# Performance work log

Measured on AMD Instinct MI355X. Metric: run time of the kernel, lower is better.

The kernel has to match this reference:

```python
import jax, jax.numpy as jnp
import numpy as np

N, C, K = 200000, 128, 27  # active voxels, channels, 3x3x3 kernel taps
EPS = 1e-5  # torch LayerNorm default


def setup_inputs() -> dict:
    key = jax.random.key(0)
    ks = jax.random.split(key, 8)
    feats = jax.random.normal(ks[0], (N, C), dtype=jnp.float32)
    # plan-based gather map: neighbor row index per voxel per kernel tap
    neighbor_idx = jax.random.randint(ks[1], (N, K), 0, N, dtype=jnp.int32)
    # sparse conv weights: one [C_in, C_out] slice per kernel offset
    conv_w = jax.random.normal(ks[2], (K, C, C), dtype=jnp.float32) * (1.0 / np.sqrt(K * C))
    conv_b = jax.random.normal(ks[3], (C,), dtype=jnp.float32) * 0.02
    # torch.nn.Linear(C, C): weight [out, in], y = x @ W^T + b
    lin_w = jax.random.normal(ks[4], (C, C), dtype=jnp.float32) * (1.0 / np.sqrt(C))
    lin_b = jax.random.normal(ks[5], (C,), dtype=jnp.float32) * 0.02
    ln_w = 1.0 + 0.02 * jax.random.normal(ks[6], (C,), dtype=jnp.float32)
    ln_b = 0.02 * jax.random.normal(ks[7], (C,), dtype=jnp.float32)
    return {
        "feats": feats, "neighbor_idx": neighbor_idx,
        "conv_w": conv_w, "conv_b": conv_b,
        "lin_w": lin_w, "lin_b": lin_b,
        "ln_w": ln_w, "ln_b": ln_b,
    }


def _sparse_conv(feats, neighbor_idx, conv_w, conv_b):
    # Stream over the 27 kernel taps: gather [N,C] then GEMM with the tap's
    # [C,C] slice; never materialize the [N,27,C] gathered tensor.
    def step(acc, tap):
        idx_k, w_k = tap  # idx_k: [N], w_k: [C, C]
        return acc + feats[idx_k] @ w_k, None

    acc0 = jnp.zeros((feats.shape[0], conv_w.shape[2]), dtype=feats.dtype)
    out, _ = jax.lax.scan(step, acc0, (neighbor_idx.T, conv_w))
    return out + conv_b


def reference(feats, neighbor_idx, conv_w, conv_b, lin_w, lin_b, ln_w, ln_b):
    x = _sparse_conv(feats, neighbor_idx, conv_w, conv_b)   # [N, C]
    x = x @ lin_w.T + lin_b                                  # Linear
    mu = jnp.mean(x, axis=-1, keepdims=True)                 # LayerNorm
    var = jnp.mean(jnp.square(x - mu), axis=-1, keepdims=True)
    x = (x - mu) * jax.lax.rsqrt(var + EPS) * ln_w + ln_b
    return x
```

## Files before the change

### kernel.cpp

```cpp
#include <hip/hip_runtime.h>
#include <hip/hip_bf16.h>
#include <stdint.h>

#define N_ROWS 200000
#define C_DIM  128
#define TAPS   27
#define EPS    1e-5f

typedef __attribute__((ext_vector_type(8)))  short  short8;
typedef __attribute__((ext_vector_type(16))) float  floatx16;

#if __has_builtin(__builtin_amdgcn_make_buffer_rsrc) && __has_builtin(__builtin_amdgcn_raw_buffer_load_b128)
#define GATHER_SC0 1
#else
#define GATHER_SC0 0
#endif

__device__ __forceinline__ unsigned int f2bf(float f) {
  union { float f; unsigned int u; } v; v.f = f;
  unsigned int r = v.u + 0x7FFFu + ((v.u >> 16) & 1u);
  return r >> 16;
}

__device__ __forceinline__ void glds16(const unsigned short* g, unsigned short* l) {
  __builtin_amdgcn_global_load_lds(
      (const __attribute__((address_space(1))) unsigned int*)g,
      (__attribute__((address_space(3))) unsigned int*)l, 16, 0, 0);
}

#if GATHER_SC0
__device__ __forceinline__ short8 ld16sc0(__amdgpu_buffer_rsrc_t r, int voff) {
  return __builtin_bit_cast(short8,
      __builtin_amdgcn_raw_buffer_load_b128(r, voff, 0, 1));
}
#endif

__global__ __launch_bounds__(256) void k_cast(const float* __restrict__ in,
                                              unsigned short* __restrict__ out, int n8) {
  int i = blockIdx.x * 256 + threadIdx.x;
  if (i >= n8) return;
  const float4* p = (const float4*)in + (size_t)i * 2;
  float4 a = p[0], b = p[1];
  uint4 v;
  v.x = f2bf(a.x) | (f2bf(a.y) << 16);
  v.y = f2bf(a.z) | (f2bf(a.w) << 16);
  v.z = f2bf(b.x) | (f2bf(b.y) << 16);
  v.w = f2bf(b.z) | (f2bf(b.w) << 16);
  *(uint4*)(out + (size_t)i * 8) = v;
}

__global__ __launch_bounds__(256) void k_tr(const int* __restrict__ in,
                                            int* __restrict__ outT) {
  __shared__ int t[1728];
  const int tile = blockIdx.x;
  const int* src = in + (size_t)tile * 1728;
  for (int e = threadIdx.x; e < 1728; e += 256) t[e] = src[e];
  __syncthreads();
  const int base = tile * 64;
  for (int o = threadIdx.x; o < 1728; o += 256) {
    int k = o >> 6, r = o & 63;
    outT[(size_t)k * N_ROWS + base + r] = t[r * 27 + k];
  }
}

__global__ __launch_bounds__(256) void k_fold(const float* __restrict__ conv_w,
                                              const float* __restrict__ lin_w,
                                              const float* __restrict__ conv_b,
                                              const float* __restrict__ lin_b,
                                              unsigned short* __restrict__ wfrag,
                                              float* __restrict__ biasf) {
  __shared__ float lwT[128 * 128];
  for (int e = threadIdx.x; e < 16384; e += 256) {
    int co = e >> 7, t = e & 127;
    lwT[t * 128 + (co ^ (t & 31))] = lin_w[e];
  }
  __syncthreads();

  int id = blockIdx.x * 256 + threadIdx.x;
  const int NW = TAPS * 4 * 8 * 64;
  if (id < NW) {
    int l  = id & 63;
    int s  = (id >> 6) & 7;
    int nt = (id >> 9) & 3;
    int k  = id >> 11;
    int ci0 = s * 16 + (l >> 5) * 8;
    int co  = nt * 32 + (l & 31);
    const float* cw = conv_w + ((size_t)(k * 128 + ci0)) * 128;
    float acc[8] = {0, 0, 0, 0, 0, 0, 0, 0};
    for (int t = 0; t < 128; ++t) {
      float lv = lwT[t * 128 + (co ^ (t & 31))];
#pragma unroll
      for (int j = 0; j < 8; ++j) acc[j] += cw[j * 128 + t] * lv;
    }
    uint4 v;
    v.x = f2bf(acc[0]) | (f2bf(acc[1]) << 16);
    v.y = f2bf(acc[2]) | (f2bf(acc[3]) << 16);
    v.z = f2bf(acc[4]) | (f2bf(acc[5]) << 16);
    v.w = f2bf(acc[6]) | (f2bf(acc[7]) << 16);
    *(uint4*)(wfrag + (size_t)id * 8) = v;
  } else if (id < NW + 128) {
    int co = id - NW;
    float s = lin_b[co];
    for (int t = 0; t < 128; ++t) s += conv_b[t] * lwT[t * 128 + (co ^ (t & 31))];
    biasf[co] = s;
  }
}

__global__ __launch_bounds__(512, 4) void k_main(const unsigned short* __restrict__ featsB,
                                                 const int* __restrict__ ntab,
                                                 const int nrs, const int nts,
                                                 const unsigned short* __restrict__ wfrag,
                                                 const float* __restrict__ biasf,
                                                 const float* __restrict__ lnw,
                                                 const float* __restrict__ lnb,
                                                 float* __restrict__ out) {
  __shared__ unsigned short ldsB[2][16384];

  const int tid = threadIdx.x;
  const int l   = tid & 63;
  const int w   = tid >> 6;
  const int l31 = l & 31;
  const int lh  = l >> 5;
  const int row0w = blockIdx.x * 256 + w * 32;
  const int gr  = row0w + l31;
  const int grc = (gr < N_ROWS) ? gr : 0;
  const int* np = ntab + (size_t)grc * nrs;

#if GATHER_SC0
  __amdgpu_buffer_rsrc_t rsrc = __builtin_amdgcn_make_buffer_rsrc(
      (void*)featsB, (short)0, N_ROWS * C_DIM * 2, 0x00020000);
#endif

  floatx16 acc0 = {0.f}, acc1 = {0.f}, acc2 = {0.f}, acc3 = {0.f};

  {
    const unsigned short* src = wfrag + (size_t)tid * 8;
    unsigned short* dst = &ldsB[0][w * 512];
#pragma unroll
    for (int r = 0; r < 4; ++r) glds16(src + r * 4096, dst + r * 4096);
  }
  int nid = np[0];

  for (int k = 0; k < TAPS; ++k) {
    const int cur = k & 1;
    if (k + 1 < TAPS) {
      const unsigned short* src = wfrag + (size_t)(k + 1) * 16384 + (size_t)tid * 8;
      unsigned short* dst = &ldsB[cur ^ 1][w * 512];
#pragma unroll
      for (int r = 0; r < 4; ++r) glds16(src + r * 4096, dst + r * 4096);
      __builtin_amdgcn_s_waitcnt(0xF74);
    } else {
      __builtin_amdgcn_s_waitcnt(0xF70);
    }
    __builtin_amdgcn_s_barrier();

#if GATHER_SC0
    const int voff = ((int)(unsigned)nid << 8) + (lh << 4);
    short8 a0 = ld16sc0(rsrc, voff);
    short8 a1 = ld16sc0(rsrc, voff + 32);
    short8 a2 = ld16sc0(rsrc, voff + 64);
    short8 a3 = ld16sc0(rsrc, voff + 96);
    short8 a4 = ld16sc0(rsrc, voff + 128);
    short8 a5 = ld16sc0(rsrc, voff + 160);
    short8 a6 = ld16sc0(rsrc, voff + 192);
    short8 a7 = ld16sc0(rsrc, voff + 224);
#else
    const short8* ap = (const short8*)(featsB + (size_t)(unsigned)nid * 128 + lh * 8);
    short8 a0 = ap[0],  a1 = ap[2],  a2 = ap[4],  a3 = ap[6];
    short8 a4 = ap[8],  a5 = ap[10], a6 = ap[12], a7 = ap[14];
#endif
    int nid_next = (k + 1 < TAPS) ? np[(k + 1) * nts] : 0;

    const unsigned short* bb = &ldsB[cur][l * 8];
#pragma unroll
    for (int s = 0; s < 8; ++s) {
      short8 av = (s == 0) ? a0 : (s == 1) ? a1 : (s == 2) ? a2 : (s == 3) ? a3
                : (s == 4) ? a4 : (s == 5) ? a5 : (s == 6) ? a6 : a7;
      short8 b0 = *(const short8*)(bb + (0 * 8 + s) * 512);
      short8 b1 = *(const short8*)(bb + (1 * 8 + s) * 512);
      short8 b2 = *(const short8*)(bb + (2 * 8 + s) * 512);
      short8 b3 = *(const short8*)(bb + (3 * 8 + s) * 512);
      acc0 = __builtin_amdgcn_mfma_f32_32x32x16_bf16(av, b0, acc0, 0, 0, 0);
      acc1 = __builtin_amdgcn_mfma_f32_32x32x16_bf16(av, b1, acc1, 0, 0, 0);
      acc2 = __builtin_amdgcn_mfma_f32_32x32x16_bf16(av, b2, acc2, 0, 0, 0);
      acc3 = __builtin_amdgcn_mfma_f32_32x32x16_bf16(av, b3, acc3, 0, 0, 0);
    }
    __builtin_amdgcn_s_barrier();
    nid = nid_next;
  }

  float b0 = biasf[l31], b1 = biasf[32 + l31], b2 = biasf[64 + l31], b3 = biasf[96 + l31];
  float g0 = lnw[l31],   g1 = lnw[32 + l31],   g2 = lnw[64 + l31],   g3 = lnw[96 + l31];
  float c0 = lnb[l31],   c1 = lnb[32 + l31],   c2 = lnb[64 + l31],   c3 = lnb[96 + l31];

#pragma unroll
  for (int r = 0; r < 16; ++r) {
    float x0 = acc0[r] + b0, x1 = acc1[r] + b1, x2 = acc2[r] + b2, x3 = acc3[r] + b3;
    float s = x0 + x1 + x2 + x3;
    float q = x0 * x0 + x1 * x1 + x2 * x2 + x3 * x3;
#pragma unroll
    for (int off = 16; off >= 1; off >>= 1) {
      s += __shfl_xor(s, off, 64);
      q += __shfl_xor(q, off, 64);
    }
    float mu  = s * (1.0f / 128.0f);
    float var = q * (1.0f / 128.0f) - mu * mu;
    float rs  = rsqrtf(var + EPS);
    int row   = (r & 3) + 8 * (r >> 2) + 4 * lh;
    int grow  = row0w + row;
    if (grow < N_ROWS) {
      float* o = out + (size_t)grow * 128;
      o[l31]      = (x0 - mu) * rs * g0 + c0;
      o[32 + l31] = (x1 - mu) * rs * g1 + c1;
      o[64 + l31] = (x2 - mu) * rs * g2 + c2;
      o[96 + l31] = (x3 - mu) * rs * g3 + c3;
    }
  }
}

extern "C" void kernel_launch(void* const* d_in, const int* in_sizes, int n_in,
                              void* d_out, int out_size, void* d_ws, size_t ws_size,
                              hipStream_t stream) {
  const float* feats  = (const float*)d_in[0];
  const int*   nidx   = (const int*)d_in[1];
  const float* conv_w = (const float*)d_in[2];
  const float* conv_b = (const float*)d_in[3];
  const float* lin_w  = (const float*)d_in[4];
  const float* lin_b  = (const float*)d_in[5];
  const float* ln_w   = (const float*)d_in[6];
  const float* ln_b   = (const float*)d_in[7];
  float* out = (float*)d_out;

  unsigned short* featsB = (unsigned short*)d_ws;
  unsigned short* wfrag  = (unsigned short*)((char*)d_ws + 51200000);
  float*          biasf  = (float*)((char*)d_ws + 51200000 + 884736);
  int*            nidxT  = (int*)((char*)d_ws + 51200000 + 884736 + 512);

  const size_t ws_need_tr = 51200000ULL + 884736ULL + 512ULL + 21600000ULL;
  const bool use_tr = (ws_size >= ws_need_tr);

  int n8 = N_ROWS * C_DIM / 8;
  k_cast<<<(n8 + 255) / 256, 256, 0, stream>>>(feats, featsB, n8);
  k_fold<<<(TAPS * 2048 + 128 + 255) / 256, 256, 0, stream>>>(conv_w, lin_w, conv_b, lin_b,
                                                              wfrag, biasf);
  if (use_tr) k_tr<<<N_ROWS / 64, 256, 0, stream>>>(nidx, nidxT);

  k_main<<<(N_ROWS + 255) / 256, 512, 0, stream>>>(
      featsB,
      use_tr ? (const int*)nidxT : nidx,
      use_tr ? 1 : TAPS,
      use_tr ? N_ROWS : 1,
      wfrag, biasf, ln_w, ln_b, out);
}
```

Before: 511.7 us.

## Shrink main block to 4 waves and stream half-tap weight slices through LDS

The main kernel drops from 512 to 256 threads per block (128 rows per block), and the weight fragments are reorganized into half-tap chunks (K split into two halves of 64) so each LDS buffer holds 16 KB instead of 32 KB. The tap loop now alternates between two half-buffers, prefetching the next half while computing the current one, with explicit sched_barriers around the s_barriers. The aim is to cut LDS footprint so more blocks fit per CU and to overlap weight loads with MFMA work. In exchange each block does twice as many barriers per tap, and weight traffic per row doubles because blocks are smaller.

```diff
diff --git a/kernel.cpp b/kernel.cpp
--- a/kernel.cpp
+++ b/kernel.cpp
@@ -15,6 +15,9 @@
 #else
 #define GATHER_SC0 0
 #endif
+
+#define SBAR()  __builtin_amdgcn_s_barrier()
+#define SCHED() __builtin_amdgcn_sched_barrier(0)
 
 __device__ __forceinline__ unsigned int f2bf(float f) {
   union { float f; unsigned int u; } v; v.f = f;
@@ -77,12 +80,14 @@
   __syncthreads();
 
   int id = blockIdx.x * 256 + threadIdx.x;
-  const int NW = TAPS * 4 * 8 * 64;
+  const int NW = TAPS * 2 * 4 * 4 * 64;
   if (id < NW) {
     int l  = id & 63;
-    int s  = (id >> 6) & 7;
-    int nt = (id >> 9) & 3;
+    int sh = (id >> 6) & 3;
+    int nt = (id >> 8) & 3;
+    int h  = (id >> 10) & 1;
     int k  = id >> 11;
+    int s  = h * 4 + sh;
     int ci0 = s * 16 + (l >> 5) * 8;
     int co  = nt * 32 + (l & 31);
     const float* cw = conv_w + ((size_t)(k * 128 + ci0)) * 128;
@@ -106,7 +111,7 @@
   }
 }
 
-__global__ __launch_bounds__(512, 4) void k_main(const unsigned short* __restrict__ featsB,
+__global__ __launch_bounds__(256, 4) void k_main(const unsigned short* __restrict__ featsB,
                                                  const int* __restrict__ ntab,
                                                  const int nrs, const int nts,
                                                  const unsigned short* __restrict__ wfrag,
@@ -114,14 +119,14 @@
                                                  const float* __restrict__ lnw,
                                                  const float* __restrict__ lnb,
                                                  float* __restrict__ out) {
-  __shared__ unsigned short ldsB[2][16384];
+  __shared__ unsigned short ldsB[2][8192];
 
   const int tid = threadIdx.x;
   const int l   = tid & 63;
   const int w   = tid >> 6;
   const int l31 = l & 31;
   const int lh  = l >> 5;
-  const int row0w = blockIdx.x * 256 + w * 32;
+  const int row0w = blockIdx.x * 128 + w * 32;
   const int gr  = row0w + l31;
   const int grc = (gr < N_ROWS) ? gr : 0;
   const int* np = ntab + (size_t)grc * nrs;
@@ -137,55 +142,89 @@
     const unsigned short* src = wfrag + (size_t)tid * 8;
     unsigned short* dst = &ldsB[0][w * 512];
 #pragma unroll
-    for (int r = 0; r < 4; ++r) glds16(src + r * 4096, dst + r * 4096);
+    for (int r = 0; r < 4; ++r) glds16(src + r * 2048, dst + r * 2048);
   }
   int nid = np[0];
-
-  for (int k = 0; k < TAPS; ++k) {
-    const int cur = k & 1;
-    if (k + 1 < TAPS) {
-      const unsigned short* src = wfrag + (size_t)(k + 1) * 16384 + (size_t)tid * 8;
-      unsigned short* dst = &ldsB[cur ^ 1][w * 512];
-#pragma unroll
-      for (int r = 0; r < 4; ++r) glds16(src + r * 4096, dst + r * 4096);
-      __builtin_amdgcn_s_waitcnt(0xF74);
-    } else {
-      __builtin_amdgcn_s_waitcnt(0xF70);
-    }
-    __builtin_amdgcn_s_barrier();
+  short8 a0, a1, a2, a3, a4, a5, a6, a7;
+
+  for (int t = 0; t < TAPS; ++t) {
+    {
+      const unsigned short* src = wfrag + (size_t)(2 * t + 1) * 8192 + (size_t)tid * 8;
+      unsigned short* dst = &ldsB[1][w * 512];
+#pragma unroll
+      for (int r = 0; r < 4; ++r) glds16(src + r * 2048, dst + r * 2048);
+    }
+    SCHED();
+    __builtin_amdgcn_s_waitcnt(0xF74);
+    SCHED();
+    SBAR();
+    SCHED();
 
 #if GATHER_SC0
     const int voff = ((int)(unsigned)nid << 8) + (lh << 4);
-    short8 a0 = ld16sc0(rsrc, voff);
-    short8 a1 = ld16sc0(rsrc, voff + 32);
-    short8 a2 = ld16sc0(rsrc, voff + 64);
-    short8 a3 = ld16sc0(rsrc, voff + 96);
-    short8 a4 = ld16sc0(rsrc, voff + 128);
-    short8 a5 = ld16sc0(rsrc, voff + 160);
-    short8 a6 = ld16sc0(rsrc, voff + 192);
-    short8 a7 = ld16sc0(rsrc, voff + 224);
+    a0 = ld16sc0(rsrc, voff);
+    a1 = ld16sc0(rsrc, voff + 32);
+    a2 = ld16sc0(rsrc, voff + 64);
+    a3 = ld16sc0(rsrc, voff + 96);
+    a4 = ld16sc0(rsrc, voff + 128);
+    a5 = ld16sc0(rsrc, voff + 160);
+    a6 = ld16sc0(rsrc, voff + 192);
+    a7 = ld16sc0(rsrc, voff + 224);
 #else
     const short8* ap = (const short8*)(featsB + (size_t)(unsigned)nid * 128 + lh * 8);
-    short8 a0 = ap[0],  a1 = ap[2],  a2 = ap[4],  a3 = ap[6];
-    short8 a4 = ap[8],  a5 = ap[10], a6 = ap[12], a7 = ap[14];
-#endif
-    int nid_next = (k + 1 < TAPS) ? np[(k + 1) * nts] : 0;
-
-    const unsigned short* bb = &ldsB[cur][l * 8];
-#pragma unroll
-    for (int s = 0; s < 8; ++s) {
-      short8 av = (s == 0) ? a0 : (s == 1) ? a1 : (s == 2) ? a2 : (s == 3) ? a3
-                : (s == 4) ? a4 : (s == 5) ? a5 : (s == 6) ? a6 : a7;
-      short8 b0 = *(const short8*)(bb + (0 * 8 + s) * 512);
-      short8 b1 = *(const short8*)(bb + (1 * 8 + s) * 512);
-      short8 b2 = *(const short8*)(bb + (2 * 8 + s) * 512);
-      short8 b3 = *(const short8*)(bb + (3 * 8 + s) * 512);
-      acc0 = __builtin_amdgcn_mfma_f32_32x32x16_bf16(av, b0, acc0, 0, 0, 0);
-      acc1 = __builtin_amdgcn_mfma_f32_32x32x16_bf16(av, b1, acc1, 0, 0, 0);
-      acc2 = __builtin_amdgcn_mfma_f32_32x32x16_bf16(av, b2, acc2, 0, 0, 0);
-      acc3 = __builtin_amdgcn_mfma_f32_32x32x16_bf16(av, b3, acc3, 0, 0, 0);
-    }
-    __builtin_amdgcn_s_barrier();
+    a0 = ap[0];  a1 = ap[2];  a2 = ap[4];  a3 = ap[6];
+    a4 = ap[8];  a5 = ap[10]; a6 = ap[12]; a7 = ap[14];
+#endif
+    int nid_next = (t + 1 < TAPS) ? np[(t + 1) * nts] : 0;
+
+    {
+      const unsigned short* bb = &ldsB[0][l * 8];
+#pragma unroll
+      for (int sh = 0; sh < 4; ++sh) {
+        short8 av = (sh == 0) ? a0 : (sh == 1) ? a1 : (sh == 2) ? a2 : a3;
+        short8 b0 = *(const short8*)(bb + (0 * 4 + sh) * 512);
+        short8 b1 = *(const short8*)(bb + (1 * 4 + sh) * 512);
+        short8 b2 = *(const short8*)(bb + (2 * 4 + sh) * 512);
+        short8 b3 = *(const short8*)(bb + (3 * 4 + sh) * 512);
+        acc0 = __builtin_amdgcn_mfma_f32_32x32x16_bf16(av, b0, acc0, 0, 0, 0);
+        acc1 = __builtin_amdgcn_mfma_f32_32x32x16_bf16(av, b1, acc1, 0, 0, 0);
+        acc2 = __builtin_amdgcn_mfma_f32_32x32x16_bf16(av, b2, acc2, 0, 0, 0);
+        acc3 = __builtin_amdgcn_mfma_f32_32x32x16_bf16(av, b3, acc3, 0, 0, 0);
+      }
+    }
+    SCHED();
+    SBAR();
+    SCHED();
+
+    if (t + 1 < TAPS) {
+      const unsigned short* src = wfrag + (size_t)(2 * t + 2) * 8192 + (size_t)tid * 8;
+      unsigned short* dst = &ldsB[0][w * 512];
+#pragma unroll
+      for (int r = 0; r < 4; ++r) glds16(src + r * 2048, dst + r * 2048);
+    }
+    SCHED();
+    SBAR();
+    SCHED();
+    {
+      const unsigned short* bb = &ldsB[1][l * 8];
+#pragma unroll
+      for (int sh = 0; sh < 4; ++sh) {
+        short8 av = (sh == 0) ? a4 : (sh == 1) ? a5 : (sh == 2) ? a6 : a7;
+        short8 b0 = *(const short8*)(bb + (0 * 4 + sh) * 512);
+        short8 b1 = *(const short8*)(bb + (1 * 4 + sh) * 512);
+        short8 b2 = *(const short8*)(bb + (2 * 4 + sh) * 512);
+        short8 b3 = *(const short8*)(bb + (3 * 4 + sh) * 512);
+        acc0 = __builtin_amdgcn_mfma_f32_32x32x16_bf16(av, b0, acc0, 0, 0, 0);
+        acc1 = __builtin_amdgcn_mfma_f32_32x32x16_bf16(av, b1, acc1, 0, 0, 0);
+        acc2 = __builtin_amdgcn_mfma_f32_32x32x16_bf16(av, b2, acc2, 0, 0, 0);
+        acc3 = __builtin_amdgcn_mfma_f32_32x32x16_bf16(av, b3, acc3, 0, 0, 0);
+      }
+    }
+    if (t + 1 < TAPS) {
+      SCHED();
+      SBAR();
+      SCHED();
+    }
     nid = nid_next;
   }
 
@@ -245,7 +284,7 @@
                                                               wfrag, biasf);
   if (use_tr) k_tr<<<N_ROWS / 64, 256, 0, stream>>>(nidx, nidxT);
 
-  k_main<<<(N_ROWS + 255) / 256, 512, 0, stream>>>(
+  k_main<<<(N_ROWS + 127) / 128, 256, 0, stream>>>(
       featsB,
       use_tr ? (const int*)nidxT : nidx,
       use_tr ? 1 : TAPS,
```

After: 481.0 us. -6.0%, faster.
